# Performance work log

Measured on AMD Instinct MI355X. Metric: run time of the kernel, lower is better.

Reference implementation:

```python
import jax, jax.numpy as jnp
import numpy as np

WALL_COT = 0.5   # init kwarg wall_cot
N_SEG = 64       # number of distinct segment ids (matches fill_max of segs)
MIN_FRAC = 0.01  # thresholds used in the torch loop


def _nearest_ds(x, He, We):
    """F.interpolate(x, size=(He,We), mode='nearest').squeeze(1) for x:[B,1,H,W].
    torch nearest picks src index floor(dst * H/He)."""
    B, _, H, W = x.shape
    iy = (jnp.arange(He) * H) // He
    ix = (jnp.arange(We) * W) // We
    return x[:, 0][:, iy][:, :, ix]  # [B,He,We]


def setup_inputs() -> dict:
    key = jax.random.key(0)
    ks = jax.random.split(key, 6)
    B, C_img, H, W = 8, 3, 512, 512
    C_feat, He, We = 64, 128, 128
    return {
        "outputs": jax.random.normal(ks[0], (B, C_img, H, W), dtype=jnp.float32),
        "inputs": jax.random.normal(ks[1], (B, C_img, H, W), dtype=jnp.float32),
        "enc1": jax.random.normal(ks[2], (B, C_feat, He, We), dtype=jnp.float32),
        "dec1": jax.random.normal(ks[3], (B, C_feat, He, We), dtype=jnp.float32),
        "masks": jax.random.uniform(ks[4], (B, 1, H, W), dtype=jnp.float32),
        "segs": jax.random.randint(ks[5], (B, 1, H, W), 0, N_SEG, dtype=jnp.int32),
        "confidence": jnp.zeros((1,), dtype=jnp.float32),
        "iteration": 1,
        "epoch": 0,
    }


def reference(outputs, inputs, enc1, dec1, masks, segs, confidence, iteration, epoch):
    B, _, He, We = enc1.shape
    npix = He * We

    # nearest-neighbor downsample of segment ids and cost masks to feature res
    seg_i = _nearest_ds(segs, He, We)            # [B,He,We] int
    mask_i = _nearest_ds(masks, He, We)          # [B,He,We]

    # per-pixel reconstruction error, mean over channels
    reco_error = jnp.mean((enc1 - dec1) ** 2, axis=1)  # [B,He,We]

    # segmented reductions: offset segment ids per batch item -> one flat pass
    flat_seg = (jnp.arange(B, dtype=jnp.int32)[:, None] * N_SEG
                + seg_i.reshape(B, -1)).reshape(-1)       # [B*He*We]
    f32 = reco_error.dtype
    counts = jax.ops.segment_sum(jnp.ones_like(flat_seg, dtype=f32), flat_seg,
                                 num_segments=B * N_SEG)  # [B*N_SEG]
    sum_err = jax.ops.segment_sum(reco_error.reshape(-1), flat_seg,
                                  num_segments=B * N_SEG)
    pos_px = ((mask_i > 0) & (mask_i < WALL_COT)).reshape(-1).astype(f32)
    pos_cnt = jax.ops.segment_sum(pos_px, flat_seg, num_segments=B * N_SEG)

    safe_cnt = jnp.maximum(counts, 1.0)
    mean_err = sum_err / safe_cnt                  # mean reco error per segment
    valid = (counts / npix) >= MIN_FRAC            # torch: skip if count frac < 0.01
    pos_flag = (pos_cnt / safe_cnt) > MIN_FRAC     # torch: pos/counts > 0.01
    sel = (valid & pos_flag).astype(f32)
    # flat_reco_error_pos.mean()
    flat_pos_mean = jnp.sum(mean_err * sel) / jnp.maximum(jnp.sum(sel), 1.0)

    # recovery loss: zero-out targets where mask >= wall_cot, masked mean
    targets = jnp.where(masks >= WALL_COT, jnp.zeros_like(inputs), inputs)  # bcast [B,1,H,W]
    mse_recov = jnp.sum((outputs - targets) ** 2, axis=1, keepdims=True)    # [B,1,H,W]
    m = (masks > 0).astype(f32)
    loss_recov = jnp.sum(mse_recov * m) / jnp.maximum(jnp.sum(m), 1.0)

    return loss_recov + flat_pos_mean
```

## Files before the change

kernel.cpp:

```cpp
#include <hip/hip_runtime.h>
#include <stdint.h>

#define BATCH   8
#define CIMG    3
#define HFULL   512
#define WFULL   512
#define HWFULL  (HFULL * WFULL)
#define CFEAT   64
#define HE      128
#define WE      128
#define HWE     (HE * WE)
#define NSEG    64
#define NBSEG   (BATCH * NSEG)
#define WALL_COT 0.5f
#define MIN_FRAC 0.01f

#define NBLK    2048
#define NREP    8

#define WS_BINS_FLOATS (NREP * 3 * NBSEG)
#define WS_BNUM  WS_BINS_FLOATS
#define WS_BDEN  (WS_BINS_FLOATS + NBLK)
#define WS_ZERO_FLOATS WS_BINS_FLOATS

#define KEEPF4(v) asm volatile("" :: "v"((v).x), "v"((v).y), "v"((v).z), "v"((v).w))

typedef uint32_t u32g __attribute__((address_space(1)));
typedef uint32_t u32l __attribute__((address_space(3)));

__global__ __launch_bounds__(256, 2) void confloss_main_kernel(
    const float* __restrict__ outputs, const float* __restrict__ inputs,
    const float* __restrict__ enc1,    const float* __restrict__ dec1,
    const float* __restrict__ masks,   const int* __restrict__ segs,
    float* __restrict__ ws)
{
    const int tid = threadIdx.x;
    const int w   = tid >> 6;
    const int l   = tid & 63;
    const int i   = blockIdx.x * 256 + tid;

    __shared__ float sA[4][8][256];
    __shared__ float s_sumW[4][NSEG];
    __shared__ float s_cnt[NSEG], s_pos[NSEG];
    __shared__ float s_rn[4], s_rd[4];

    s_sumW[w][l] = 0.f;
    if (tid < NSEG) { s_cnt[tid] = 0.f; s_pos[tid] = 0.f; }
    __syncthreads();

    const int g  = i & 32767;
    const int c  = i >> 15;
    const int ba = g >> 12;
    const int ra = (g & 4095) * 4;
    const size_t abase = ((size_t)ba * CFEAT + (size_t)c * 4) * HWE + ra;
    const float* ep = enc1 + abase;
    const float* dp = dec1 + abase;

#if __has_builtin(__builtin_amdgcn_global_load_lds)
#pragma unroll
    for (int k = 0; k < 4; ++k)
        __builtin_amdgcn_global_load_lds((const u32g*)(ep + (size_t)k * HWE),
                                         (u32l*)(&sA[w][k][0]), 16, 0, 0);
#pragma unroll
    for (int k = 0; k < 4; ++k)
        __builtin_amdgcn_global_load_lds((const u32g*)(dp + (size_t)k * HWE),
                                         (u32l*)(&sA[w][4 + k][0]), 16, 0, 0);
#else
#pragma unroll
    for (int k = 0; k < 4; ++k) {
        *(float4*)&sA[w][k][l * 4]     = *(const float4*)(ep + (size_t)k * HWE);
        *(float4*)&sA[w][4 + k][l * 4] = *(const float4*)(dp + (size_t)k * HWE);
    }
#endif

    const int bb = i >> 16;
    const int rb = (i & 65535) * 4;
    const float* ob = outputs + (size_t)bb * (CIMG * HWFULL) + rb;
    const float* ib = inputs  + (size_t)bb * (CIMG * HWFULL) + rb;
    const float4 mB = *(const float4*)(masks + (size_t)bb * HWFULL + rb);
    const float4 o0 = *(const float4*)(ob);
    const float4 o1 = *(const float4*)(ob + HWFULL);
    const float4 o2 = *(const float4*)(ob + 2 * HWFULL);
    const float4 i0 = *(const float4*)(ib);
    const float4 i1 = *(const float4*)(ib + HWFULL);
    const float4 i2 = *(const float4*)(ib + 2 * HWFULL);

    const int ya = ra >> 7, xa = ra & (WE - 1);
    const int fb = ba * HWFULL + (ya * 4) * WFULL + xa * 4;
    const int s0 = segs[fb], s1 = segs[fb + 4], s2 = segs[fb + 8], s3 = segs[fb + 12];
    const bool duty = (c == (g & 15));
    float mk0 = 1.f, mk1 = 1.f, mk2 = 1.f, mk3 = 1.f;
    if (duty) {
        mk0 = masks[fb];     mk1 = masks[fb + 4];
        mk2 = masks[fb + 8]; mk3 = masks[fb + 12];
    }

    KEEPF4(mB); KEEPF4(o0); KEEPF4(o1); KEEPF4(o2);
    KEEPF4(i0); KEEPF4(i1); KEEPF4(i2);
    asm volatile("" :: "v"(s0), "v"(s1), "v"(s2), "v"(s3));
    asm volatile("s_waitcnt vmcnt(0)" ::: "memory");

    float num = 0.f, den = 0.f;
    {
        float tgt, dd, mse;
        mse = 0.f;
        tgt = (mB.x >= WALL_COT) ? 0.f : i0.x; dd = o0.x - tgt; mse += dd * dd;
        tgt = (mB.x >= WALL_COT) ? 0.f : i1.x; dd = o1.x - tgt; mse += dd * dd;
        tgt = (mB.x >= WALL_COT) ? 0.f : i2.x; dd = o2.x - tgt; mse += dd * dd;
        if (mB.x > 0.f) { num += mse; den += 1.f; }
        mse = 0.f;
        tgt = (mB.y >= WALL_COT) ? 0.f : i0.y; dd = o0.y - tgt; mse += dd * dd;
        tgt = (mB.y >= WALL_COT) ? 0.f : i1.y; dd = o1.y - tgt; mse += dd * dd;
        tgt = (mB.y >= WALL_COT) ? 0.f : i2.y; dd = o2.y - tgt; mse += dd * dd;
        if (mB.y > 0.f) { num += mse; den += 1.f; }
        mse = 0.f;
        tgt = (mB.z >= WALL_COT) ? 0.f : i0.z; dd = o0.z - tgt; mse += dd * dd;
        tgt = (mB.z >= WALL_COT) ? 0.f : i1.z; dd = o1.z - tgt; mse += dd * dd;
        tgt = (mB.z >= WALL_COT) ? 0.f : i2.z; dd = o2.z - tgt; mse += dd * dd;
        if (mB.z > 0.f) { num += mse; den += 1.f; }
        mse = 0.f;
        tgt = (mB.w >= WALL_COT) ? 0.f : i0.w; dd = o0.w - tgt; mse += dd * dd;
        tgt = (mB.w >= WALL_COT) ? 0.f : i1.w; dd = o1.w - tgt; mse += dd * dd;
        tgt = (mB.w >= WALL_COT) ? 0.f : i2.w; dd = o2.w - tgt; mse += dd * dd;
        if (mB.w > 0.f) { num += mse; den += 1.f; }
    }

    {
        const float4 E0 = *(const float4*)&sA[w][0][l * 4];
        const float4 E1 = *(const float4*)&sA[w][1][l * 4];
        const float4 E2 = *(const float4*)&sA[w][2][l * 4];
        const float4 E3 = *(const float4*)&sA[w][3][l * 4];
        const float4 D0 = *(const float4*)&sA[w][4][l * 4];
        const float4 D1 = *(const float4*)&sA[w][5][l * 4];
        const float4 D2 = *(const float4*)&sA[w][6][l * 4];
        const float4 D3 = *(const float4*)&sA[w][7][l * 4];

        float t0, t1, t2, t3;
        t0 = E0.x - D0.x; t1 = E1.x - D1.x; t2 = E2.x - D2.x; t3 = E3.x - D3.x;
        const float p0 = (t0*t0 + t1*t1 + t2*t2 + t3*t3) * (1.0f / (float)CFEAT);
        t0 = E0.y - D0.y; t1 = E1.y - D1.y; t2 = E2.y - D2.y; t3 = E3.y - D3.y;
        const float p1 = (t0*t0 + t1*t1 + t2*t2 + t3*t3) * (1.0f / (float)CFEAT);
        t0 = E0.z - D0.z; t1 = E1.z - D1.z; t2 = E2.z - D2.z; t3 = E3.z - D3.z;
        const float p2 = (t0*t0 + t1*t1 + t2*t2 + t3*t3) * (1.0f / (float)CFEAT);
        t0 = E0.w - D0.w; t1 = E1.w - D1.w; t2 = E2.w - D2.w; t3 = E3.w - D3.w;
        const float p3 = (t0*t0 + t1*t1 + t2*t2 + t3*t3) * (1.0f / (float)CFEAT);

        atomicAdd(&s_sumW[w][s0], p0);
        atomicAdd(&s_sumW[w][s1], p1);
        atomicAdd(&s_sumW[w][s2], p2);
        atomicAdd(&s_sumW[w][s3], p3);
        if (duty) {
            atomicAdd(&s_cnt[s0], 1.f); if (mk0 > 0.f && mk0 < WALL_COT) atomicAdd(&s_pos[s0], 1.f);
            atomicAdd(&s_cnt[s1], 1.f); if (mk1 > 0.f && mk1 < WALL_COT) atomicAdd(&s_pos[s1], 1.f);
            atomicAdd(&s_cnt[s2], 1.f); if (mk2 > 0.f && mk2 < WALL_COT) atomicAdd(&s_pos[s2], 1.f);
            atomicAdd(&s_cnt[s3], 1.f); if (mk3 > 0.f && mk3 < WALL_COT) atomicAdd(&s_pos[s3], 1.f);
        }
    }

#pragma unroll
    for (int off = 32; off >= 1; off >>= 1) {
        num += __shfl_down(num, off);
        den += __shfl_down(den, off);
    }
    if (l == 0) { s_rn[w] = num; s_rd[w] = den; }
    __syncthreads();

    if (tid == 0) {
        ws[WS_BNUM + blockIdx.x] = s_rn[0] + s_rn[1] + s_rn[2] + s_rn[3];
        ws[WS_BDEN + blockIdx.x] = s_rd[0] + s_rd[1] + s_rd[2] + s_rd[3];
    }
    if (tid < NSEG) {
        const int rep  = blockIdx.x & (NREP - 1);
        float* bins = ws + rep * (3 * NBSEG);
        const int gb = ba * NSEG + tid;
        const float sv = s_sumW[0][tid] + s_sumW[1][tid] + s_sumW[2][tid] + s_sumW[3][tid];
        if (sv != 0.f) atomicAdd(&bins[NBSEG + gb], sv);
        const float cv = s_cnt[tid];
        if (cv != 0.f) atomicAdd(&bins[gb], cv);
        const float pv = s_pos[tid];
        if (pv != 0.f) atomicAdd(&bins[2 * NBSEG + gb], pv);
    }
}

__global__ __launch_bounds__(512) void confloss_finalize_kernel(
    const float* __restrict__ ws, float* __restrict__ out)
{
    const int t = threadIdx.x;
    float rn = 0.f, rd = 0.f;
#pragma unroll
    for (int k = 0; k < NBLK / 512; ++k) {
        rn += ws[WS_BNUM + t + k * 512];
        rd += ws[WS_BDEN + t + k * 512];
    }
    float cnt = 0.f, sum = 0.f, pos = 0.f;
#pragma unroll
    for (int rep = 0; rep < NREP; ++rep) {
        const float* bins = ws + rep * (3 * NBSEG);
        cnt += bins[t];
        sum += bins[NBSEG + t];
        pos += bins[2 * NBSEG + t];
    }
    const float safe = fmaxf(cnt, 1.0f);
    const float mean = sum / safe;
    const bool valid = (cnt / (float)HWE) >= MIN_FRAC;
    const bool posf  = (pos / safe) > MIN_FRAC;
    float sel = (valid && posf) ? 1.0f : 0.0f;
    float val = mean * sel;

#pragma unroll
    for (int off = 32; off >= 1; off >>= 1) {
        val += __shfl_down(val, off);
        sel += __shfl_down(sel, off);
        rn  += __shfl_down(rn,  off);
        rd  += __shfl_down(rd,  off);
    }
    __shared__ float sv[8], ss[8], sn[8], sd[8];
    const int wid = t >> 6;
    if ((t & 63) == 0) { sv[wid] = val; ss[wid] = sel; sn[wid] = rn; sd[wid] = rd; }
    __syncthreads();
    if (t == 0) {
        float tv = 0.f, ts = 0.f, tn = 0.f, td = 0.f;
#pragma unroll
        for (int w = 0; w < 8; ++w) { tv += sv[w]; ts += ss[w]; tn += sn[w]; td += sd[w]; }
        const float flat_pos_mean = tv / fmaxf(ts, 1.0f);
        const float loss_recov = tn / fmaxf(td, 1.0f);
        out[0] = loss_recov + flat_pos_mean;
    }
}

extern "C" void kernel_launch(void* const* d_in, const int* in_sizes, int n_in,
                              void* d_out, int out_size, void* d_ws, size_t ws_size,
                              hipStream_t stream) {
    const float* outputs = (const float*)d_in[0];
    const float* inputs  = (const float*)d_in[1];
    const float* enc1    = (const float*)d_in[2];
    const float* dec1    = (const float*)d_in[3];
    const float* masks   = (const float*)d_in[4];
    const int*   segs    = (const int*)d_in[5];
    float* ws  = (float*)d_ws;
    float* out = (float*)d_out;

    hipMemsetAsync(ws, 0, WS_ZERO_FLOATS * sizeof(float), stream);

    confloss_main_kernel<<<NBLK, 256, 0, stream>>>(
        outputs, inputs, enc1, dec1, masks, segs, ws);
    confloss_finalize_kernel<<<1, 512, 0, stream>>>(ws, out);
}
```

Baseline: 37.95 us.

## Precompute packed downsampled seg/mask ids in a pre-kernel, drop LDS staging

Adds a pre-kernel that gathers the nearest-downsampled segment ids and positive-mask flags into a packed int array in the workspace, and also zeroes the bins, replacing the memset. In the main kernel, every thread used to do strided gathers of segs and masks. Now each reads one contiguous int4. The enc1/dec1 loads go straight to registers instead of being staged through LDS with global_load_lds, which frees shared memory and may raise occupancy. In exchange it adds an extra kernel launch and a serial dependency between the two kernels.

Result: no change. 37.30 us (-1.7%).

```diff
diff --git a/kernel.cpp b/kernel.cpp
--- a/kernel.cpp
+++ b/kernel.cpp
@@ -20,13 +20,28 @@
 
 #define WS_BINS_FLOATS (NREP * 3 * NBSEG)
 #define WS_BNUM  WS_BINS_FLOATS
-#define WS_BDEN  (WS_BINS_FLOATS + NBLK)
+#define WS_BDEN  (WS_BNUM + NBLK)
+#define WS_SEGDS (WS_BDEN + NBLK)
 #define WS_ZERO_FLOATS WS_BINS_FLOATS
 
 #define KEEPF4(v) asm volatile("" :: "v"((v).x), "v"((v).y), "v"((v).z), "v"((v).w))
-
-typedef uint32_t u32g __attribute__((address_space(1)));
-typedef uint32_t u32l __attribute__((address_space(3)));
+#define KEEPI4(v) asm volatile("" :: "v"((v).x), "v"((v).y), "v"((v).z), "v"((v).w))
+
+__global__ __launch_bounds__(256) void confloss_pre_kernel(
+    const float* __restrict__ masks, const int* __restrict__ segs,
+    float* __restrict__ ws)
+{
+    const int p = blockIdx.x * 256 + threadIdx.x;
+    const int b = p >> 14;
+    const int r = p & (HWE - 1);
+    const int y = r >> 7, x = r & (WE - 1);
+    const int src = b * HWFULL + (y * 4) * WFULL + x * 4;
+    const int   seg = segs[src];
+    const float mk  = masks[src];
+    const int packed = seg | ((mk > 0.f && mk < WALL_COT) ? 256 : 0);
+    ((int*)(ws + WS_SEGDS))[p] = packed;
+    if (p < WS_ZERO_FLOATS) ws[p] = 0.f;
+}
 
 __global__ __launch_bounds__(256, 2) void confloss_main_kernel(
     const float* __restrict__ outputs, const float* __restrict__ inputs,
@@ -39,11 +54,9 @@
     const int l   = tid & 63;
     const int i   = blockIdx.x * 256 + tid;
 
-    __shared__ float sA[4][8][256];
     __shared__ float s_sumW[4][NSEG];
     __shared__ float s_cnt[NSEG], s_pos[NSEG];
     __shared__ float s_rn[4], s_rd[4];
-
     s_sumW[w][l] = 0.f;
     if (tid < NSEG) { s_cnt[tid] = 0.f; s_pos[tid] = 0.f; }
     __syncthreads();
@@ -56,27 +69,19 @@
     const float* ep = enc1 + abase;
     const float* dp = dec1 + abase;
 
-#if __has_builtin(__builtin_amdgcn_global_load_lds)
-#pragma unroll
-    for (int k = 0; k < 4; ++k)
-        __builtin_amdgcn_global_load_lds((const u32g*)(ep + (size_t)k * HWE),
-                                         (u32l*)(&sA[w][k][0]), 16, 0, 0);
-#pragma unroll
-    for (int k = 0; k < 4; ++k)
-        __builtin_amdgcn_global_load_lds((const u32g*)(dp + (size_t)k * HWE),
-                                         (u32l*)(&sA[w][4 + k][0]), 16, 0, 0);
-#else
-#pragma unroll
-    for (int k = 0; k < 4; ++k) {
-        *(float4*)&sA[w][k][l * 4]     = *(const float4*)(ep + (size_t)k * HWE);
-        *(float4*)&sA[w][4 + k][l * 4] = *(const float4*)(dp + (size_t)k * HWE);
-    }
-#endif
-
     const int bb = i >> 16;
     const int rb = (i & 65535) * 4;
     const float* ob = outputs + (size_t)bb * (CIMG * HWFULL) + rb;
     const float* ib = inputs  + (size_t)bb * (CIMG * HWFULL) + rb;
+
+    const float4 e0 = *(const float4*)(ep);
+    const float4 e1 = *(const float4*)(ep + HWE);
+    const float4 e2 = *(const float4*)(ep + 2 * HWE);
+    const float4 e3 = *(const float4*)(ep + 3 * HWE);
+    const float4 d0 = *(const float4*)(dp);
+    const float4 d1 = *(const float4*)(dp + HWE);
+    const float4 d2 = *(const float4*)(dp + 2 * HWE);
+    const float4 d3 = *(const float4*)(dp + 3 * HWE);
     const float4 mB = *(const float4*)(masks + (size_t)bb * HWFULL + rb);
     const float4 o0 = *(const float4*)(ob);
     const float4 o1 = *(const float4*)(ob + HWFULL);
@@ -84,20 +89,12 @@
     const float4 i0 = *(const float4*)(ib);
     const float4 i1 = *(const float4*)(ib + HWFULL);
     const float4 i2 = *(const float4*)(ib + 2 * HWFULL);
-
-    const int ya = ra >> 7, xa = ra & (WE - 1);
-    const int fb = ba * HWFULL + (ya * 4) * WFULL + xa * 4;
-    const int s0 = segs[fb], s1 = segs[fb + 4], s2 = segs[fb + 8], s3 = segs[fb + 12];
-    const bool duty = (c == (g & 15));
-    float mk0 = 1.f, mk1 = 1.f, mk2 = 1.f, mk3 = 1.f;
-    if (duty) {
-        mk0 = masks[fb];     mk1 = masks[fb + 4];
-        mk2 = masks[fb + 8]; mk3 = masks[fb + 12];
-    }
-
+    const int4 pk = *(const int4*)(((const int*)(ws + WS_SEGDS)) + 4 * g);
+
+    KEEPF4(e0); KEEPF4(e1); KEEPF4(e2); KEEPF4(e3);
+    KEEPF4(d0); KEEPF4(d1); KEEPF4(d2); KEEPF4(d3);
     KEEPF4(mB); KEEPF4(o0); KEEPF4(o1); KEEPF4(o2);
-    KEEPF4(i0); KEEPF4(i1); KEEPF4(i2);
-    asm volatile("" :: "v"(s0), "v"(s1), "v"(s2), "v"(s3));
+    KEEPF4(i0); KEEPF4(i1); KEEPF4(i2); KEEPI4(pk);
     asm volatile("s_waitcnt vmcnt(0)" ::: "memory");
 
     float num = 0.f, den = 0.f;
@@ -126,34 +123,26 @@
     }
 
     {
-        const float4 E0 = *(const float4*)&sA[w][0][l * 4];
-        const float4 E1 = *(const float4*)&sA[w][1][l * 4];
-        const float4 E2 = *(const float4*)&sA[w][2][l * 4];
-        const float4 E3 = *(const float4*)&sA[w][3][l * 4];
-        const float4 D0 = *(const float4*)&sA[w][4][l * 4];
-        const float4 D1 = *(const float4*)&sA[w][5][l * 4];
-        const float4 D2 = *(const float4*)&sA[w][6][l * 4];
-        const float4 D3 = *(const float4*)&sA[w][7][l * 4];
-
+        const int s0 = pk.x & 255, s1 = pk.y & 255, s2 = pk.z & 255, s3 = pk.w & 255;
         float t0, t1, t2, t3;
-        t0 = E0.x - D0.x; t1 = E1.x - D1.x; t2 = E2.x - D2.x; t3 = E3.x - D3.x;
+        t0 = e0.x - d0.x; t1 = e1.x - d1.x; t2 = e2.x - d2.x; t3 = e3.x - d3.x;
         const float p0 = (t0*t0 + t1*t1 + t2*t2 + t3*t3) * (1.0f / (float)CFEAT);
-        t0 = E0.y - D0.y; t1 = E1.y - D1.y; t2 = E2.y - D2.y; t3 = E3.y - D3.y;
+        t0 = e0.y - d0.y; t1 = e1.y - d1.y; t2 = e2.y - d2.y; t3 = e3.y - d3.y;
         const float p1 = (t0*t0 + t1*t1 + t2*t2 + t3*t3) * (1.0f / (float)CFEAT);
-        t0 = E0.z - D0.z; t1 = E1.z - D1.z; t2 = E2.z - D2.z; t3 = E3.z - D3.z;
+        t0 = e0.z - d0.z; t1 = e1.z - d1.z; t2 = e2.z - d2.z; t3 = e3.z - d3.z;
         const float p2 = (t0*t0 + t1*t1 + t2*t2 + t3*t3) * (1.0f / (float)CFEAT);
-        t0 = E0.w - D0.w; t1 = E1.w - D1.w; t2 = E2.w - D2.w; t3 = E3.w - D3.w;
+        t0 = e0.w - d0.w; t1 = e1.w - d1.w; t2 = e2.w - d2.w; t3 = e3.w - d3.w;
         const float p3 = (t0*t0 + t1*t1 + t2*t2 + t3*t3) * (1.0f / (float)CFEAT);
 
         atomicAdd(&s_sumW[w][s0], p0);
         atomicAdd(&s_sumW[w][s1], p1);
         atomicAdd(&s_sumW[w][s2], p2);
         atomicAdd(&s_sumW[w][s3], p3);
-        if (duty) {
-            atomicAdd(&s_cnt[s0], 1.f); if (mk0 > 0.f && mk0 < WALL_COT) atomicAdd(&s_pos[s0], 1.f);
-            atomicAdd(&s_cnt[s1], 1.f); if (mk1 > 0.f && mk1 < WALL_COT) atomicAdd(&s_pos[s1], 1.f);
-            atomicAdd(&s_cnt[s2], 1.f); if (mk2 > 0.f && mk2 < WALL_COT) atomicAdd(&s_pos[s2], 1.f);
-            atomicAdd(&s_cnt[s3], 1.f); if (mk3 > 0.f && mk3 < WALL_COT) atomicAdd(&s_pos[s3], 1.f);
+        if (c == (g & 15)) {
+            atomicAdd(&s_cnt[s0], 1.f); if (pk.x & 256) atomicAdd(&s_pos[s0], 1.f);
+            atomicAdd(&s_cnt[s1], 1.f); if (pk.y & 256) atomicAdd(&s_pos[s1], 1.f);
+            atomicAdd(&s_cnt[s2], 1.f); if (pk.z & 256) atomicAdd(&s_pos[s2], 1.f);
+            atomicAdd(&s_cnt[s3], 1.f); if (pk.w & 256) atomicAdd(&s_pos[s3], 1.f);
         }
     }
 
@@ -170,7 +159,7 @@
         ws[WS_BDEN + blockIdx.x] = s_rd[0] + s_rd[1] + s_rd[2] + s_rd[3];
     }
     if (tid < NSEG) {
-        const int rep  = blockIdx.x & (NREP - 1);
+        const int rep = blockIdx.x & (NREP - 1);
         float* bins = ws + rep * (3 * NBSEG);
         const int gb = ba * NSEG + tid;
         const float sv = s_sumW[0][tid] + s_sumW[1][tid] + s_sumW[2][tid] + s_sumW[3][tid];
@@ -240,8 +229,7 @@
     float* ws  = (float*)d_ws;
     float* out = (float*)d_out;
 
-    hipMemsetAsync(ws, 0, WS_ZERO_FLOATS * sizeof(float), stream);
-
+    confloss_pre_kernel<<<(BATCH * HWE) / 256, 256, 0, stream>>>(masks, segs, ws);
     confloss_main_kernel<<<NBLK, 256, 0, stream>>>(
         outputs, inputs, enc1, dec1, masks, segs, ws);
     confloss_finalize_kernel<<<1, 512, 0, stream>>>(ws, out);
```

## Halve block count, process two work items per thread with direct register loads

Applied to the files above, without the earlier changes.

Halves the grid so each thread handles two channel groups of enc/dec (c and c+32) and two batch items of the recovery loss. The LDS staging through global_load_lds is replaced by direct vector loads into registers. The duty condition is widened to match the new mapping. This aims to raise memory-level parallelism per thread and cut per-block overhead and atomic traffic, at the cost of more registers and the removal of the occupancy hint.

After: 36.99 us (median of 2 runs). -2.5%, faster.

```diff
diff --git a/kernel.cpp b/kernel.cpp
--- a/kernel.cpp
+++ b/kernel.cpp
@@ -15,20 +15,17 @@
 #define WALL_COT 0.5f
 #define MIN_FRAC 0.01f
 
-#define NBLK    2048
+#define NBLK    1024
 #define NREP    8
 
 #define WS_BINS_FLOATS (NREP * 3 * NBSEG)
 #define WS_BNUM  WS_BINS_FLOATS
-#define WS_BDEN  (WS_BINS_FLOATS + NBLK)
+#define WS_BDEN  (WS_BNUM + NBLK)
 #define WS_ZERO_FLOATS WS_BINS_FLOATS
 
-#define KEEPF4(v) asm volatile("" :: "v"((v).x), "v"((v).y), "v"((v).z), "v"((v).w))
-
-typedef uint32_t u32g __attribute__((address_space(1)));
-typedef uint32_t u32l __attribute__((address_space(3)));
-
-__global__ __launch_bounds__(256, 2) void confloss_main_kernel(
+typedef float vf4 __attribute__((ext_vector_type(4)));
+
+__global__ __launch_bounds__(256) void confloss_main_kernel(
     const float* __restrict__ outputs, const float* __restrict__ inputs,
     const float* __restrict__ enc1,    const float* __restrict__ dec1,
     const float* __restrict__ masks,   const int* __restrict__ segs,
@@ -39,11 +36,9 @@
     const int l   = tid & 63;
     const int i   = blockIdx.x * 256 + tid;
 
-    __shared__ float sA[4][8][256];
     __shared__ float s_sumW[4][NSEG];
     __shared__ float s_cnt[NSEG], s_pos[NSEG];
     __shared__ float s_rn[4], s_rd[4];
-
     s_sumW[w][l] = 0.f;
     if (tid < NSEG) { s_cnt[tid] = 0.f; s_pos[tid] = 0.f; }
     __syncthreads();
@@ -53,98 +48,114 @@
     const int ba = g >> 12;
     const int ra = (g & 4095) * 4;
     const size_t abase = ((size_t)ba * CFEAT + (size_t)c * 4) * HWE + ra;
-    const float* ep = enc1 + abase;
-    const float* dp = dec1 + abase;
-
-#if __has_builtin(__builtin_amdgcn_global_load_lds)
-#pragma unroll
-    for (int k = 0; k < 4; ++k)
-        __builtin_amdgcn_global_load_lds((const u32g*)(ep + (size_t)k * HWE),
-                                         (u32l*)(&sA[w][k][0]), 16, 0, 0);
-#pragma unroll
-    for (int k = 0; k < 4; ++k)
-        __builtin_amdgcn_global_load_lds((const u32g*)(dp + (size_t)k * HWE),
-                                         (u32l*)(&sA[w][4 + k][0]), 16, 0, 0);
-#else
-#pragma unroll
-    for (int k = 0; k < 4; ++k) {
-        *(float4*)&sA[w][k][l * 4]     = *(const float4*)(ep + (size_t)k * HWE);
-        *(float4*)&sA[w][4 + k][l * 4] = *(const float4*)(dp + (size_t)k * HWE);
-    }
-#endif
+    const float* ep0 = enc1 + abase;
+    const float* dp0 = dec1 + abase;
+    const float* ep1 = ep0 + (size_t)32 * HWE;
+    const float* dp1 = dp0 + (size_t)32 * HWE;
 
     const int bb = i >> 16;
     const int rb = (i & 65535) * 4;
-    const float* ob = outputs + (size_t)bb * (CIMG * HWFULL) + rb;
-    const float* ib = inputs  + (size_t)bb * (CIMG * HWFULL) + rb;
-    const float4 mB = *(const float4*)(masks + (size_t)bb * HWFULL + rb);
-    const float4 o0 = *(const float4*)(ob);
-    const float4 o1 = *(const float4*)(ob + HWFULL);
-    const float4 o2 = *(const float4*)(ob + 2 * HWFULL);
-    const float4 i0 = *(const float4*)(ib);
-    const float4 i1 = *(const float4*)(ib + HWFULL);
-    const float4 i2 = *(const float4*)(ib + 2 * HWFULL);
+    const float* ob0 = outputs + (size_t)bb * (CIMG * HWFULL) + rb;
+    const float* ib0 = inputs  + (size_t)bb * (CIMG * HWFULL) + rb;
+    const float* ob1 = ob0 + (size_t)4 * (CIMG * HWFULL);
+    const float* ib1 = ib0 + (size_t)4 * (CIMG * HWFULL);
+    const float* mp0 = masks + (size_t)bb * HWFULL + rb;
+    const float* mp1 = mp0 + (size_t)4 * HWFULL;
 
     const int ya = ra >> 7, xa = ra & (WE - 1);
     const int fb = ba * HWFULL + (ya * 4) * WFULL + xa * 4;
+    const int gl = g & 15;
+    const bool duty = (gl == c) || (gl == c + 8);
+
+    const vf4 e00 = *(const vf4*)(ep0);
+    const vf4 e01 = *(const vf4*)(ep0 + HWE);
+    const vf4 e02 = *(const vf4*)(ep0 + 2 * HWE);
+    const vf4 e03 = *(const vf4*)(ep0 + 3 * HWE);
+    const vf4 d00 = *(const vf4*)(dp0);
+    const vf4 d01 = *(const vf4*)(dp0 + HWE);
+    const vf4 d02 = *(const vf4*)(dp0 + 2 * HWE);
+    const vf4 d03 = *(const vf4*)(dp0 + 3 * HWE);
+    const vf4 mB0 = *(const vf4*)(mp0);
+    const vf4 o00 = *(const vf4*)(ob0);
+    const vf4 o01 = *(const vf4*)(ob0 + HWFULL);
+    const vf4 o02 = *(const vf4*)(ob0 + 2 * HWFULL);
+    const vf4 i00 = *(const vf4*)(ib0);
+    const vf4 i01 = *(const vf4*)(ib0 + HWFULL);
+    const vf4 i02 = *(const vf4*)(ib0 + 2 * HWFULL);
     const int s0 = segs[fb], s1 = segs[fb + 4], s2 = segs[fb + 8], s3 = segs[fb + 12];
-    const bool duty = (c == (g & 15));
     float mk0 = 1.f, mk1 = 1.f, mk2 = 1.f, mk3 = 1.f;
     if (duty) {
         mk0 = masks[fb];     mk1 = masks[fb + 4];
         mk2 = masks[fb + 8]; mk3 = masks[fb + 12];
     }
-
-    KEEPF4(mB); KEEPF4(o0); KEEPF4(o1); KEEPF4(o2);
-    KEEPF4(i0); KEEPF4(i1); KEEPF4(i2);
-    asm volatile("" :: "v"(s0), "v"(s1), "v"(s2), "v"(s3));
-    asm volatile("s_waitcnt vmcnt(0)" ::: "memory");
+    asm volatile("" ::
+        "v"(e00), "v"(e01), "v"(e02), "v"(e03),
+        "v"(d00), "v"(d01), "v"(d02), "v"(d03),
+        "v"(mB0), "v"(o00), "v"(o01), "v"(o02),
+        "v"(i00), "v"(i01), "v"(i02));
+    asm volatile("" :: "v"(s0), "v"(s1), "v"(s2), "v"(s3),
+                       "v"(mk0), "v"(mk1), "v"(mk2), "v"(mk3));
+
+    const vf4 e10 = *(const vf4*)(ep1);
+    const vf4 e11 = *(const vf4*)(ep1 + HWE);
+    const vf4 e12 = *(const vf4*)(ep1 + 2 * HWE);
+    const vf4 e13 = *(const vf4*)(ep1 + 3 * HWE);
+    const vf4 d10 = *(const vf4*)(dp1);
+    const vf4 d11 = *(const vf4*)(dp1 + HWE);
+    const vf4 d12 = *(const vf4*)(dp1 + 2 * HWE);
+    const vf4 d13 = *(const vf4*)(dp1 + 3 * HWE);
+    const vf4 mB1 = *(const vf4*)(mp1);
+    const vf4 o10 = *(const vf4*)(ob1);
+    const vf4 o11 = *(const vf4*)(ob1 + HWFULL);
+    const vf4 o12 = *(const vf4*)(ob1 + 2 * HWFULL);
+    const vf4 i10 = *(const vf4*)(ib1);
+    const vf4 i11 = *(const vf4*)(ib1 + HWFULL);
+    const vf4 i12 = *(const vf4*)(ib1 + 2 * HWFULL);
+    asm volatile("" ::
+        "v"(e10), "v"(e11), "v"(e12), "v"(e13),
+        "v"(d10), "v"(d11), "v"(d12), "v"(d13),
+        "v"(mB1), "v"(o10), "v"(o11), "v"(o12),
+        "v"(i10), "v"(i11), "v"(i12));
 
     float num = 0.f, den = 0.f;
+#define BPIX(mv, a0, a1, a2, b0, b1, b2)                                   \
+    {                                                                       \
+        float tgt, dd, mse = 0.f;                                           \
+        tgt = ((mv) >= WALL_COT) ? 0.f : (b0); dd = (a0) - tgt; mse += dd*dd; \
+        tgt = ((mv) >= WALL_COT) ? 0.f : (b1); dd = (a1) - tgt; mse += dd*dd; \
+        tgt = ((mv) >= WALL_COT) ? 0.f : (b2); dd = (a2) - tgt; mse += dd*dd; \
+        if ((mv) > 0.f) { num += mse; den += 1.f; }                         \
+    }
+    BPIX(mB0.x, o00.x, o01.x, o02.x, i00.x, i01.x, i02.x)
+    BPIX(mB0.y, o00.y, o01.y, o02.y, i00.y, i01.y, i02.y)
+    BPIX(mB0.z, o00.z, o01.z, o02.z, i00.z, i01.z, i02.z)
+    BPIX(mB0.w, o00.w, o01.w, o02.w, i00.w, i01.w, i02.w)
+    BPIX(mB1.x, o10.x, o11.x, o12.x, i10.x, i11.x, i12.x)
+    BPIX(mB1.y, o10.y, o11.y, o12.y, i10.y, i11.y, i12.y)
+    BPIX(mB1.z, o10.z, o11.z, o12.z, i10.z, i11.z, i12.z)
+    BPIX(mB1.w, o10.w, o11.w, o12.w, i10.w, i11.w, i12.w)
+#undef BPIX
+
     {
-        float tgt, dd, mse;
-        mse = 0.f;
-        tgt = (mB.x >= WALL_COT) ? 0.f : i0.x; dd = o0.x - tgt; mse += dd * dd;
-        tgt = (mB.x >= WALL_COT) ? 0.f : i1.x; dd = o1.x - tgt; mse += dd * dd;
-        tgt = (mB.x >= WALL_COT) ? 0.f : i2.x; dd = o2.x - tgt; mse += dd * dd;
-        if (mB.x > 0.f) { num += mse; den += 1.f; }
-        mse = 0.f;
-        tgt = (mB.y >= WALL_COT) ? 0.f : i0.y; dd = o0.y - tgt; mse += dd * dd;
-        tgt = (mB.y >= WALL_COT) ? 0.f : i1.y; dd = o1.y - tgt; mse += dd * dd;
-        tgt = (mB.y >= WALL_COT) ? 0.f : i2.y; dd = o2.y - tgt; mse += dd * dd;
-        if (mB.y > 0.f) { num += mse; den += 1.f; }
-        mse = 0.f;
-        tgt = (mB.z >= WALL_COT) ? 0.f : i0.z; dd = o0.z - tgt; mse += dd * dd;
-        tgt = (mB.z >= WALL_COT) ? 0.f : i1.z; dd = o1.z - tgt; mse += dd * dd;
-        tgt = (mB.z >= WALL_COT) ? 0.f : i2.z; dd = o2.z - tgt; mse += dd * dd;
-        if (mB.z > 0.f) { num += mse; den += 1.f; }
-        mse = 0.f;
-        tgt = (mB.w >= WALL_COT) ? 0.f : i0.w; dd = o0.w - tgt; mse += dd * dd;
-        tgt = (mB.w >= WALL_COT) ? 0.f : i1.w; dd = o1.w - tgt; mse += dd * dd;
-        tgt = (mB.w >= WALL_COT) ? 0.f : i2.w; dd = o2.w - tgt; mse += dd * dd;
-        if (mB.w > 0.f) { num += mse; den += 1.f; }
-    }
-
-    {
-        const float4 E0 = *(const float4*)&sA[w][0][l * 4];
-        const float4 E1 = *(const float4*)&sA[w][1][l * 4];
-        const float4 E2 = *(const float4*)&sA[w][2][l * 4];
-        const float4 E3 = *(const float4*)&sA[w][3][l * 4];
-        const float4 D0 = *(const float4*)&sA[w][4][l * 4];
-        const float4 D1 = *(const float4*)&sA[w][5][l * 4];
-        const float4 D2 = *(const float4*)&sA[w][6][l * 4];
-        const float4 D3 = *(const float4*)&sA[w][7][l * 4];
-
-        float t0, t1, t2, t3;
-        t0 = E0.x - D0.x; t1 = E1.x - D1.x; t2 = E2.x - D2.x; t3 = E3.x - D3.x;
-        const float p0 = (t0*t0 + t1*t1 + t2*t2 + t3*t3) * (1.0f / (float)CFEAT);
-        t0 = E0.y - D0.y; t1 = E1.y - D1.y; t2 = E2.y - D2.y; t3 = E3.y - D3.y;
-        const float p1 = (t0*t0 + t1*t1 + t2*t2 + t3*t3) * (1.0f / (float)CFEAT);
-        t0 = E0.z - D0.z; t1 = E1.z - D1.z; t2 = E2.z - D2.z; t3 = E3.z - D3.z;
-        const float p2 = (t0*t0 + t1*t1 + t2*t2 + t3*t3) * (1.0f / (float)CFEAT);
-        t0 = E0.w - D0.w; t1 = E1.w - D1.w; t2 = E2.w - D2.w; t3 = E3.w - D3.w;
-        const float p3 = (t0*t0 + t1*t1 + t2*t2 + t3*t3) * (1.0f / (float)CFEAT);
-
+        float t0, t1, t2, t3, u0, u1, u2, u3;
+#define APIX(f)                                                             \
+        t0 = e00.f - d00.f; t1 = e01.f - d01.f;                             \
+        t2 = e02.f - d02.f; t3 = e03.f - d03.f;                             \
+        u0 = e10.f - d10.f; u1 = e11.f - d11.f;                             \
+        u2 = e12.f - d12.f; u3 = e13.f - d13.f;
+        APIX(x)
+        const float p0 = (t0*t0 + t1*t1 + t2*t2 + t3*t3 +
+                          u0*u0 + u1*u1 + u2*u2 + u3*u3) * (1.0f / (float)CFEAT);
+        APIX(y)
+        const float p1 = (t0*t0 + t1*t1 + t2*t2 + t3*t3 +
+                          u0*u0 + u1*u1 + u2*u2 + u3*u3) * (1.0f / (float)CFEAT);
+        APIX(z)
+        const float p2 = (t0*t0 + t1*t1 + t2*t2 + t3*t3 +
+                          u0*u0 + u1*u1 + u2*u2 + u3*u3) * (1.0f / (float)CFEAT);
+        APIX(w)
+        const float p3 = (t0*t0 + t1*t1 + t2*t2 + t3*t3 +
+                          u0*u0 + u1*u1 + u2*u2 + u3*u3) * (1.0f / (float)CFEAT);
+#undef APIX
         atomicAdd(&s_sumW[w][s0], p0);
         atomicAdd(&s_sumW[w][s1], p1);
         atomicAdd(&s_sumW[w][s2], p2);
@@ -170,7 +181,7 @@
         ws[WS_BDEN + blockIdx.x] = s_rd[0] + s_rd[1] + s_rd[2] + s_rd[3];
     }
     if (tid < NSEG) {
-        const int rep  = blockIdx.x & (NREP - 1);
+        const int rep = blockIdx.x & (NREP - 1);
         float* bins = ws + rep * (3 * NBSEG);
         const int gb = ba * NSEG + tid;
         const float sv = s_sumW[0][tid] + s_sumW[1][tid] + s_sumW[2][tid] + s_sumW[3][tid];
@@ -221,7 +232,7 @@
     if (t == 0) {
         float tv = 0.f, ts = 0.f, tn = 0.f, td = 0.f;
 #pragma unroll
-        for (int w = 0; w < 8; ++w) { tv += sv[w]; ts += ss[w]; tn += sn[w]; td += sd[w]; }
+        for (int k = 0; k < 8; ++k) { tv += sv[k]; ts += ss[k]; tn += sn[k]; td += sd[k]; }
         const float flat_pos_mean = tv / fmaxf(ts, 1.0f);
         const float loss_recov = tn / fmaxf(td, 1.0f);
         out[0] = loss_recov + flat_pos_mean;
```

## Process four tiles per thread with double-buffered register loads and fewer blocks

Applied to the files above, without the earlier changes.

The grid shrinks from 2048 to 512 blocks. Each thread now walks four channel/batch steps, using two register buffer sets so the loads for the next step are in flight while the current step is computed. The LDS staging of enc/dec via global_load_lds and the explicit vmcnt(0) wait are dropped in favour of direct vector loads into registers. Count and positive bins become per-wave to match the per-wave sum bins. The aim is more memory-level parallelism per thread and less per-block overhead, at the cost of high VGPR use and fewer resident waves per CU.

Measured after the change: 39.66 us. 4.5% more time.

```diff
diff --git a/kernel.cpp b/kernel.cpp
--- a/kernel.cpp
+++ b/kernel.cpp
@@ -15,18 +15,81 @@
 #define WALL_COT 0.5f
 #define MIN_FRAC 0.01f
 
-#define NBLK    2048
+#define NBLK    512
 #define NREP    8
 
 #define WS_BINS_FLOATS (NREP * 3 * NBSEG)
 #define WS_BNUM  WS_BINS_FLOATS
-#define WS_BDEN  (WS_BINS_FLOATS + NBLK)
+#define WS_BDEN  (WS_BNUM + NBLK)
 #define WS_ZERO_FLOATS WS_BINS_FLOATS
 
-#define KEEPF4(v) asm volatile("" :: "v"((v).x), "v"((v).y), "v"((v).z), "v"((v).w))
-
-typedef uint32_t u32g __attribute__((address_space(1)));
-typedef uint32_t u32l __attribute__((address_space(3)));
+typedef float vf4 __attribute__((ext_vector_type(4)));
+
+#define ISSUE(S)                                                        \
+    e##S##0 = *(const vf4*)(ep);                                        \
+    e##S##1 = *(const vf4*)(ep + HWE);                                  \
+    e##S##2 = *(const vf4*)(ep + 2 * HWE);                              \
+    e##S##3 = *(const vf4*)(ep + 3 * HWE);                              \
+    d##S##0 = *(const vf4*)(dp);                                        \
+    d##S##1 = *(const vf4*)(dp + HWE);                                  \
+    d##S##2 = *(const vf4*)(dp + 2 * HWE);                              \
+    d##S##3 = *(const vf4*)(dp + 3 * HWE);                              \
+    m##S    = *(const vf4*)(mpp);                                       \
+    o##S##0 = *(const vf4*)(obp);                                       \
+    o##S##1 = *(const vf4*)(obp + HWFULL);                              \
+    o##S##2 = *(const vf4*)(obp + 2 * HWFULL);                          \
+    q##S##0 = *(const vf4*)(ibp);                                       \
+    q##S##1 = *(const vf4*)(ibp + HWFULL);                              \
+    q##S##2 = *(const vf4*)(ibp + 2 * HWFULL);                          \
+    asm volatile("" ::                                                  \
+        "v"(e##S##0), "v"(e##S##1), "v"(e##S##2), "v"(e##S##3),         \
+        "v"(d##S##0), "v"(d##S##1), "v"(d##S##2), "v"(d##S##3),         \
+        "v"(m##S), "v"(o##S##0), "v"(o##S##1), "v"(o##S##2),            \
+        "v"(q##S##0), "v"(q##S##1), "v"(q##S##2));                      \
+    __builtin_amdgcn_sched_barrier(0);                                  \
+    ep  += (size_t)16 * HWE;  dp  += (size_t)16 * HWE;                  \
+    obp += (size_t)2 * CIMG * HWFULL;                                   \
+    ibp += (size_t)2 * CIMG * HWFULL;                                   \
+    mpp += (size_t)2 * HWFULL;
+
+#define BPIX(mv, a0, a1, a2, b0, b1, b2)                                \
+    {                                                                   \
+        float tgt, dd, mse = 0.f;                                       \
+        tgt = ((mv) >= WALL_COT) ? 0.f : (b0); dd = (a0) - tgt; mse += dd*dd; \
+        tgt = ((mv) >= WALL_COT) ? 0.f : (b1); dd = (a1) - tgt; mse += dd*dd; \
+        tgt = ((mv) >= WALL_COT) ? 0.f : (b2); dd = (a2) - tgt; mse += dd*dd; \
+        if ((mv) > 0.f) { num += mse; den += 1.f; }                     \
+    }
+
+#define CONSUME(S)                                                      \
+    {                                                                   \
+        const vf4 Xm  = m##S;                                           \
+        const vf4 Xo0 = o##S##0, Xo1 = o##S##1, Xo2 = o##S##2;          \
+        const vf4 Xq0 = q##S##0, Xq1 = q##S##1, Xq2 = q##S##2;          \
+        const vf4 Xe0 = e##S##0, Xe1 = e##S##1, Xe2 = e##S##2, Xe3 = e##S##3; \
+        const vf4 Xd0 = d##S##0, Xd1 = d##S##1, Xd2 = d##S##2, Xd3 = d##S##3; \
+        BPIX(Xm.x, Xo0.x, Xo1.x, Xo2.x, Xq0.x, Xq1.x, Xq2.x)            \
+        BPIX(Xm.y, Xo0.y, Xo1.y, Xo2.y, Xq0.y, Xq1.y, Xq2.y)            \
+        BPIX(Xm.z, Xo0.z, Xo1.z, Xo2.z, Xq0.z, Xq1.z, Xq2.z)            \
+        BPIX(Xm.w, Xo0.w, Xo1.w, Xo2.w, Xq0.w, Xq1.w, Xq2.w)            \
+        float t0, t1, t2, t3;                                           \
+        t0 = Xe0.x - Xd0.x; t1 = Xe1.x - Xd1.x;                         \
+        t2 = Xe2.x - Xd2.x; t3 = Xe3.x - Xd3.x;                         \
+        const float p0 = (t0*t0 + t1*t1 + t2*t2 + t3*t3) * (1.0f / (float)CFEAT); \
+        t0 = Xe0.y - Xd0.y; t1 = Xe1.y - Xd1.y;                         \
+        t2 = Xe2.y - Xd2.y; t3 = Xe3.y - Xd3.y;                         \
+        const float p1 = (t0*t0 + t1*t1 + t2*t2 + t3*t3) * (1.0f / (float)CFEAT); \
+        t0 = Xe0.z - Xd0.z; t1 = Xe1.z - Xd1.z;                         \
+        t2 = Xe2.z - Xd2.z; t3 = Xe3.z - Xd3.z;                         \
+        const float p2 = (t0*t0 + t1*t1 + t2*t2 + t3*t3) * (1.0f / (float)CFEAT); \
+        t0 = Xe0.w - Xd0.w; t1 = Xe1.w - Xd1.w;                         \
+        t2 = Xe2.w - Xd2.w; t3 = Xe3.w - Xd3.w;                         \
+        const float p3 = (t0*t0 + t1*t1 + t2*t2 + t3*t3) * (1.0f / (float)CFEAT); \
+        atomicAdd(&s_sumW[w][s0], p0);                                  \
+        atomicAdd(&s_sumW[w][s1], p1);                                  \
+        atomicAdd(&s_sumW[w][s2], p2);                                  \
+        atomicAdd(&s_sumW[w][s3], p3);                                  \
+    }
 
 __global__ __launch_bounds__(256, 2) void confloss_main_kernel(
     const float* __restrict__ outputs, const float* __restrict__ inputs,
@@ -37,124 +100,55 @@
     const int tid = threadIdx.x;
     const int w   = tid >> 6;
     const int l   = tid & 63;
-    const int i   = blockIdx.x * 256 + tid;
-
-    __shared__ float sA[4][8][256];
+    const int gid = blockIdx.x * 256 + tid;
+
     __shared__ float s_sumW[4][NSEG];
-    __shared__ float s_cnt[NSEG], s_pos[NSEG];
+    __shared__ float s_cntW[4][NSEG];
+    __shared__ float s_posW[4][NSEG];
     __shared__ float s_rn[4], s_rd[4];
-
-    s_sumW[w][l] = 0.f;
-    if (tid < NSEG) { s_cnt[tid] = 0.f; s_pos[tid] = 0.f; }
-    __syncthreads();
-
-    const int g  = i & 32767;
-    const int c  = i >> 15;
+    s_sumW[w][l] = 0.f; s_cntW[w][l] = 0.f; s_posW[w][l] = 0.f;
+
+    const int g  = gid & 32767;
+    const int c0 = gid >> 15;
     const int ba = g >> 12;
     const int ra = (g & 4095) * 4;
-    const size_t abase = ((size_t)ba * CFEAT + (size_t)c * 4) * HWE + ra;
-    const float* ep = enc1 + abase;
-    const float* dp = dec1 + abase;
-
-#if __has_builtin(__builtin_amdgcn_global_load_lds)
-#pragma unroll
-    for (int k = 0; k < 4; ++k)
-        __builtin_amdgcn_global_load_lds((const u32g*)(ep + (size_t)k * HWE),
-                                         (u32l*)(&sA[w][k][0]), 16, 0, 0);
-#pragma unroll
-    for (int k = 0; k < 4; ++k)
-        __builtin_amdgcn_global_load_lds((const u32g*)(dp + (size_t)k * HWE),
-                                         (u32l*)(&sA[w][4 + k][0]), 16, 0, 0);
-#else
-#pragma unroll
-    for (int k = 0; k < 4; ++k) {
-        *(float4*)&sA[w][k][l * 4]     = *(const float4*)(ep + (size_t)k * HWE);
-        *(float4*)&sA[w][4 + k][l * 4] = *(const float4*)(dp + (size_t)k * HWE);
-    }
-#endif
-
-    const int bb = i >> 16;
-    const int rb = (i & 65535) * 4;
-    const float* ob = outputs + (size_t)bb * (CIMG * HWFULL) + rb;
-    const float* ib = inputs  + (size_t)bb * (CIMG * HWFULL) + rb;
-    const float4 mB = *(const float4*)(masks + (size_t)bb * HWFULL + rb);
-    const float4 o0 = *(const float4*)(ob);
-    const float4 o1 = *(const float4*)(ob + HWFULL);
-    const float4 o2 = *(const float4*)(ob + 2 * HWFULL);
-    const float4 i0 = *(const float4*)(ib);
-    const float4 i1 = *(const float4*)(ib + HWFULL);
-    const float4 i2 = *(const float4*)(ib + 2 * HWFULL);
+    const int b0 = gid >> 16;
+    const int rb = (gid & 65535) * 4;
+
+    const float* ep  = enc1 + ((size_t)ba * CFEAT + (size_t)c0 * 4) * HWE + ra;
+    const float* dp  = dec1 + ((size_t)ba * CFEAT + (size_t)c0 * 4) * HWE + ra;
+    const float* obp = outputs + (size_t)b0 * (CIMG * HWFULL) + rb;
+    const float* ibp = inputs  + (size_t)b0 * (CIMG * HWFULL) + rb;
+    const float* mpp = masks   + (size_t)b0 * HWFULL + rb;
 
     const int ya = ra >> 7, xa = ra & (WE - 1);
     const int fb = ba * HWFULL + (ya * 4) * WFULL + xa * 4;
     const int s0 = segs[fb], s1 = segs[fb + 4], s2 = segs[fb + 8], s3 = segs[fb + 12];
-    const bool duty = (c == (g & 15));
+    const bool dutyA = ((g & 3) == c0);
     float mk0 = 1.f, mk1 = 1.f, mk2 = 1.f, mk3 = 1.f;
-    if (duty) {
+    if (dutyA) {
         mk0 = masks[fb];     mk1 = masks[fb + 4];
         mk2 = masks[fb + 8]; mk3 = masks[fb + 12];
     }
 
-    KEEPF4(mB); KEEPF4(o0); KEEPF4(o1); KEEPF4(o2);
-    KEEPF4(i0); KEEPF4(i1); KEEPF4(i2);
-    asm volatile("" :: "v"(s0), "v"(s1), "v"(s2), "v"(s3));
-    asm volatile("s_waitcnt vmcnt(0)" ::: "memory");
-
     float num = 0.f, den = 0.f;
-    {
-        float tgt, dd, mse;
-        mse = 0.f;
-        tgt = (mB.x >= WALL_COT) ? 0.f : i0.x; dd = o0.x - tgt; mse += dd * dd;
-        tgt = (mB.x >= WALL_COT) ? 0.f : i1.x; dd = o1.x - tgt; mse += dd * dd;
-        tgt = (mB.x >= WALL_COT) ? 0.f : i2.x; dd = o2.x - tgt; mse += dd * dd;
-        if (mB.x > 0.f) { num += mse; den += 1.f; }
-        mse = 0.f;
-        tgt = (mB.y >= WALL_COT) ? 0.f : i0.y; dd = o0.y - tgt; mse += dd * dd;
-        tgt = (mB.y >= WALL_COT) ? 0.f : i1.y; dd = o1.y - tgt; mse += dd * dd;
-        tgt = (mB.y >= WALL_COT) ? 0.f : i2.y; dd = o2.y - tgt; mse += dd * dd;
-        if (mB.y > 0.f) { num += mse; den += 1.f; }
-        mse = 0.f;
-        tgt = (mB.z >= WALL_COT) ? 0.f : i0.z; dd = o0.z - tgt; mse += dd * dd;
-        tgt = (mB.z >= WALL_COT) ? 0.f : i1.z; dd = o1.z - tgt; mse += dd * dd;
-        tgt = (mB.z >= WALL_COT) ? 0.f : i2.z; dd = o2.z - tgt; mse += dd * dd;
-        if (mB.z > 0.f) { num += mse; den += 1.f; }
-        mse = 0.f;
-        tgt = (mB.w >= WALL_COT) ? 0.f : i0.w; dd = o0.w - tgt; mse += dd * dd;
-        tgt = (mB.w >= WALL_COT) ? 0.f : i1.w; dd = o1.w - tgt; mse += dd * dd;
-        tgt = (mB.w >= WALL_COT) ? 0.f : i2.w; dd = o2.w - tgt; mse += dd * dd;
-        if (mB.w > 0.f) { num += mse; den += 1.f; }
-    }
-
-    {
-        const float4 E0 = *(const float4*)&sA[w][0][l * 4];
-        const float4 E1 = *(const float4*)&sA[w][1][l * 4];
-        const float4 E2 = *(const float4*)&sA[w][2][l * 4];
-        const float4 E3 = *(const float4*)&sA[w][3][l * 4];
-        const float4 D0 = *(const float4*)&sA[w][4][l * 4];
-        const float4 D1 = *(const float4*)&sA[w][5][l * 4];
-        const float4 D2 = *(const float4*)&sA[w][6][l * 4];
-        const float4 D3 = *(const float4*)&sA[w][7][l * 4];
-
-        float t0, t1, t2, t3;
-        t0 = E0.x - D0.x; t1 = E1.x - D1.x; t2 = E2.x - D2.x; t3 = E3.x - D3.x;
-        const float p0 = (t0*t0 + t1*t1 + t2*t2 + t3*t3) * (1.0f / (float)CFEAT);
-        t0 = E0.y - D0.y; t1 = E1.y - D1.y; t2 = E2.y - D2.y; t3 = E3.y - D3.y;
-        const float p1 = (t0*t0 + t1*t1 + t2*t2 + t3*t3) * (1.0f / (float)CFEAT);
-        t0 = E0.z - D0.z; t1 = E1.z - D1.z; t2 = E2.z - D2.z; t3 = E3.z - D3.z;
-        const float p2 = (t0*t0 + t1*t1 + t2*t2 + t3*t3) * (1.0f / (float)CFEAT);
-        t0 = E0.w - D0.w; t1 = E1.w - D1.w; t2 = E2.w - D2.w; t3 = E3.w - D3.w;
-        const float p3 = (t0*t0 + t1*t1 + t2*t2 + t3*t3) * (1.0f / (float)CFEAT);
-
-        atomicAdd(&s_sumW[w][s0], p0);
-        atomicAdd(&s_sumW[w][s1], p1);
-        atomicAdd(&s_sumW[w][s2], p2);
-        atomicAdd(&s_sumW[w][s3], p3);
-        if (duty) {
-            atomicAdd(&s_cnt[s0], 1.f); if (mk0 > 0.f && mk0 < WALL_COT) atomicAdd(&s_pos[s0], 1.f);
-            atomicAdd(&s_cnt[s1], 1.f); if (mk1 > 0.f && mk1 < WALL_COT) atomicAdd(&s_pos[s1], 1.f);
-            atomicAdd(&s_cnt[s2], 1.f); if (mk2 > 0.f && mk2 < WALL_COT) atomicAdd(&s_pos[s2], 1.f);
-            atomicAdd(&s_cnt[s3], 1.f); if (mk3 > 0.f && mk3 < WALL_COT) atomicAdd(&s_pos[s3], 1.f);
-        }
+    vf4 eA0, eA1, eA2, eA3, dA0, dA1, dA2, dA3, mA, oA0, oA1, oA2, qA0, qA1, qA2;
+    vf4 eB0, eB1, eB2, eB3, dB0, dB1, dB2, dB3, mB, oB0, oB1, oB2, qB0, qB1, qB2;
+
+    ISSUE(A)
+    ISSUE(B)
+    CONSUME(A)
+    ISSUE(A)
+    CONSUME(B)
+    ISSUE(B)
+    CONSUME(A)
+    CONSUME(B)
+
+    if (dutyA) {
+        atomicAdd(&s_cntW[w][s0], 1.f); if (mk0 > 0.f && mk0 < WALL_COT) atomicAdd(&s_posW[w][s0], 1.f);
+        atomicAdd(&s_cntW[w][s1], 1.f); if (mk1 > 0.f && mk1 < WALL_COT) atomicAdd(&s_posW[w][s1], 1.f);
+        atomicAdd(&s_cntW[w][s2], 1.f); if (mk2 > 0.f && mk2 < WALL_COT) atomicAdd(&s_posW[w][s2], 1.f);
+        atomicAdd(&s_cntW[w][s3], 1.f); if (mk3 > 0.f && mk3 < WALL_COT) atomicAdd(&s_posW[w][s3], 1.f);
     }
 
 #pragma unroll
@@ -170,14 +164,14 @@
         ws[WS_BDEN + blockIdx.x] = s_rd[0] + s_rd[1] + s_rd[2] + s_rd[3];
     }
     if (tid < NSEG) {
-        const int rep  = blockIdx.x & (NREP - 1);
+        const int rep = blockIdx.x & (NREP - 1);
         float* bins = ws + rep * (3 * NBSEG);
         const int gb = ba * NSEG + tid;
         const float sv = s_sumW[0][tid] + s_sumW[1][tid] + s_sumW[2][tid] + s_sumW[3][tid];
+        const float cv = s_cntW[0][tid] + s_cntW[1][tid] + s_cntW[2][tid] + s_cntW[3][tid];
+        const float pv = s_posW[0][tid] + s_posW[1][tid] + s_posW[2][tid] + s_posW[3][tid];
         if (sv != 0.f) atomicAdd(&bins[NBSEG + gb], sv);
-        const float cv = s_cnt[tid];
         if (cv != 0.f) atomicAdd(&bins[gb], cv);
-        const float pv = s_pos[tid];
         if (pv != 0.f) atomicAdd(&bins[2 * NBSEG + gb], pv);
     }
 }
@@ -221,7 +215,7 @@
     if (t == 0) {
         float tv = 0.f, ts = 0.f, tn = 0.f, td = 0.f;
 #pragma unroll
-        for (int w = 0; w < 8; ++w) { tv += sv[w]; ts += ss[w]; tn += sn[w]; td += sd[w]; }
+        for (int k = 0; k < 8; ++k) { tv += sv[k]; ts += ss[k]; tn += sn[k]; td += sd[k]; }
         const float flat_pos_mean = tv / fmaxf(ts, 1.0f);
         const float loss_recov = tn / fmaxf(td, 1.0f);
         out[0] = loss_recov + flat_pos_mean;
```
